# Performance work log

Hardware: AMD Instinct MI355X
Metric: run time of the kernel (lower is better)

The kernel has to match this reference:

```python
import jax, jax.numpy as jnp
import numpy as np

N = 100000
E = 1600000
IN_C, HID, HEADS, OUT_C = 128, 64, 4, 2
NEG_SLOPE = 0.2


def setup_inputs() -> dict:
    key = jax.random.key(0)
    ks = jax.random.split(key, 10)
    def glorot(k, shape):
        fan = shape[0] + shape[-1]
        return jax.random.uniform(k, shape, jnp.float32, -1.0, 1.0) * np.sqrt(6.0 / fan)
    x = jax.random.normal(ks[0], (N, IN_C), jnp.float32)
    edge_index = jax.random.randint(ks[1], (2, E), 0, N, jnp.int64)
    return {
        "x": x,
        "edge_index": edge_index,
        "W1": glorot(ks[2], (IN_C, HID)),
        "b1": jnp.zeros((HID,), jnp.float32),
        "W2": glorot(ks[3], (HID, HEADS * HID)),
        "att_src": glorot(ks[4], (HEADS, HID)) ,
        "att_dst": glorot(ks[5], (HEADS, HID)),
        "b2": jnp.zeros((HEADS * HID,), jnp.float32),
        "W3": glorot(ks[6], (HEADS * HID, OUT_C)),
        "b3": jnp.zeros((OUT_C,), jnp.float32),
    }


def _add_self_loops(edge_index, n):
    loop = jnp.arange(n, dtype=edge_index.dtype)
    src = jnp.concatenate([edge_index[0], loop])
    dst = jnp.concatenate([edge_index[1], loop])
    return src, dst


def gcn_conv(x, W, b, src, dst, n):
    # x' = X W, then symmetric deg-normalized scatter-add (self-loops included)
    xw = x @ W
    deg = jax.ops.segment_sum(jnp.ones_like(dst, dtype=xw.dtype), dst, num_segments=n)
    dinv = jnp.where(deg > 0, jax.lax.rsqrt(deg), 0.0)
    norm = dinv[src] * dinv[dst]                      # [E2]
    out = jax.ops.segment_sum(xw[src] * norm[:, None], dst, num_segments=n)
    return out + b


def gat_conv(x, W, att_src, att_dst, b, src, dst, n, heads, ch):
    xw = (x @ W).reshape(n, heads, ch)                # [N, H, C]
    a_s = (xw * att_src).sum(-1)                      # [N, H]
    a_d = (xw * att_dst).sum(-1)
    e = jax.nn.leaky_relu(a_s[src] + a_d[dst], NEG_SLOPE)   # [E2, H]
    # segment softmax over incoming edges per destination node
    m = jax.ops.segment_max(e, dst, num_segments=n)
    m = jnp.where(jnp.isfinite(m), m, 0.0)
    e = jnp.exp(e - m[dst])
    den = jax.ops.segment_sum(e, dst, num_segments=n)
    alpha = e / (den[dst] + 1e-16)                    # [E2, H]
    out = jax.ops.segment_sum(xw[src] * alpha[:, :, None], dst, num_segments=n)
    return out.reshape(n, heads * ch) + b


def reference(x, edge_index, W1, b1, W2, att_src, att_dst, b2, W3, b3):
    n = x.shape[0]
    src, dst = _add_self_loops(edge_index, n)
    h = jax.nn.relu(gcn_conv(x, W1, b1, src, dst, n))
    h = jax.nn.elu(gat_conv(h, W2, att_src, att_dst, b2, src, dst, n, HEADS, HID))
    return gcn_conv(h, W3, b3, src, dst, n)
```

## Files before the change

### kernel.cpp

```cpp
#include <hip/hip_runtime.h>
#include <math.h>

#define N_NODES 100000
#define N_EDGES 1600000
#define E2      (N_NODES + N_EDGES)
#define IN_C    128
#define HID     64
#define HEADS   4
#define HH      256
#define OUT_C   2
#define NEG_SLOPE 0.2f

#define SB   1024
#define NSB  ((N_NODES + SB - 1) / SB)
#define NCHUNK 6250
#define NRANGE 8
#define RDIV   12500
#define RT     10
#define NT1    6250
#define NGB    1563
#define NHG    (NCHUNK + NGB)

typedef __attribute__((ext_vector_type(8))) short bf16x8;
typedef __attribute__((ext_vector_type(4))) float f32x4;

__device__ __forceinline__ float bf2f(unsigned short u) {
    return __uint_as_float(((unsigned)u) << 16);
}
__device__ __forceinline__ unsigned short f2bf(float f) {
    unsigned u = __float_as_uint(f);
    u += 0x7fffu + ((u >> 16) & 1u);
    return (unsigned short)(u >> 16);
}


__global__ __launch_bounds__(256) void k_prep(const float* __restrict__ W2,
        const float* __restrict__ W1,
        const float* __restrict__ att_src, const float* __restrict__ att_dst,
        unsigned short* __restrict__ W2t, unsigned short* __restrict__ wsdt,
        unsigned short* __restrict__ W1t, int* __restrict__ cnt) {
    int b = blockIdx.x, t = threadIdx.x;
    if (b < 64) {
        int g = b * 256 + t;
        int k = g >> 8, n = g & 255;
        W2t[n * 64 + k] = f2bf(W2[g]);
        return;
    }
    if (b < 66) {
        int g = (b - 64) * 256 + t;
        wsdt[512 + g] = 0;
        int k = g >> 3, o = g & 7;
        int h = o & 3;
        const float* att = (o < 4) ? att_src : att_dst;
        float acc = 0.f;
        const float* wrow = W2 + (size_t)k * HH + h * 64;
        const float* arow = att + h * 64;
        for (int c = 0; c < 64; ++c) acc = fmaf(wrow[c], arow[c], acc);
        wsdt[o * 64 + k] = f2bf(acc);
        return;
    }
    if (b < 98) {
        int g = (b - 66) * 256 + t;
        int k = g >> 6, n = g & 63;
        W1t[n * 128 + k] = f2bf(W1[g]);
        return;
    }
    int i = ((b - 98) * 256 + t) * 4;
    if (i + 3 < N_NODES) *(int4*)(cnt + i) = make_int4(0, 0, 0, 0);
    else for (int k = 0; k < 4; ++k) if (i + k < N_NODES) cnt[i + k] = 0;
}

__global__ __launch_bounds__(256) void k_hg(const int* __restrict__ ei,
        int* __restrict__ cnt, int* __restrict__ rank,
        const float* __restrict__ x, const unsigned short* __restrict__ W1t,
        unsigned short* __restrict__ xw1b) {
    int b = blockIdx.x;
    if (b % 5 == 2) {
        int t = threadIdx.x;
        int lane = t & 63, wv = t >> 6;
        int m = lane & 15, quad = lane >> 4;
        bf16x8 B[4][4];
#pragma unroll
        for (int ct = 0; ct < 4; ++ct)
#pragma unroll
            for (int ks = 0; ks < 4; ++ks)
                B[ct][ks] = *(const bf16x8*)(W1t + (size_t)(ct * 16 + m) * IN_C
                                             + ks * 32 + quad * 8);
        int tile = (b / 5) * 4 + wv;
        if (tile >= NT1) return;
        int rbase = tile * 16;
        const float* xp = x + (size_t)(rbase + m) * IN_C + quad * 8;
        f32x4 c0 = {0.f, 0.f, 0.f, 0.f}, c1 = c0, c2 = c0, c3 = c0;
#pragma unroll
        for (int ks = 0; ks < 4; ++ks) {
            float4 f0 = *(const float4*)(xp + ks * 32);
            float4 f1 = *(const float4*)(xp + ks * 32 + 4);
            bf16x8 a;
            a[0] = (short)f2bf(f0.x); a[1] = (short)f2bf(f0.y);
            a[2] = (short)f2bf(f0.z); a[3] = (short)f2bf(f0.w);
            a[4] = (short)f2bf(f1.x); a[5] = (short)f2bf(f1.y);
            a[6] = (short)f2bf(f1.z); a[7] = (short)f2bf(f1.w);
            c0 = __builtin_amdgcn_mfma_f32_16x16x32_bf16(a, B[0][ks], c0, 0, 0, 0);
            c1 = __builtin_amdgcn_mfma_f32_16x16x32_bf16(a, B[1][ks], c1, 0, 0, 0);
            c2 = __builtin_amdgcn_mfma_f32_16x16x32_bf16(a, B[2][ks], c2, 0, 0, 0);
            c3 = __builtin_amdgcn_mfma_f32_16x16x32_bf16(a, B[3][ks], c3, 0, 0, 0);
        }
        int row0 = rbase + quad * 4;
#pragma unroll
        for (int ct = 0; ct < 4; ++ct) {
            f32x4 c = (ct == 0) ? c0 : (ct == 1) ? c1 : (ct == 2) ? c2 : c3;
            unsigned short* p = xw1b + (size_t)row0 * HID + ct * 16 + m;
#pragma unroll
            for (int r = 0; r < 4; ++r) p[(size_t)r * HID] = f2bf(c[r]);
        }
        return;
    }
    int hb = b - (b + 2) / 5;
    int i = hb * 256 + threadIdx.x;
    rank[i] = atomicAdd(&cnt[ei[N_EDGES + i]], 1);
}

__global__ __launch_bounds__(256) void k_scan1(const int* __restrict__ cnt,
                                               int* __restrict__ bsum) {
    int b = blockIdx.x, t = threadIdx.x;
    int i = b * SB + t * 4;
    int s = 0;
    if (i + 3 < N_NODES) {
        int4 v = *(const int4*)(cnt + i);
        s = (v.x + v.y) + (v.z + v.w) + 4;
    } else {
        for (int k = 0; k < 4; ++k) if (i + k < N_NODES) s += cnt[i + k] + 1;
    }
#pragma unroll
    for (int off = 1; off < 64; off <<= 1) s += __shfl_xor(s, off);
    __shared__ int wsum[4];
    int lane = t & 63, wv = t >> 6;
    if (lane == 0) wsum[wv] = s;
    __syncthreads();
    if (t == 0) bsum[b] = (wsum[0] + wsum[1]) + (wsum[2] + wsum[3]);
}

__global__ __launch_bounds__(256) void k_scan3(const int* __restrict__ cnt,
        const int* __restrict__ bsum, int* __restrict__ rowptr,
        float* __restrict__ dinv, int* __restrict__ col) {
    int b = blockIdx.x, t = threadIdx.x;
    int lane = t & 63, wv = t >> 6;
    __shared__ int wred[4];
    {
        int v = (t < b) ? bsum[t] : 0;
#pragma unroll
        for (int off = 1; off < 64; off <<= 1) v += __shfl_xor(v, off);
        if (lane == 0) wred[wv] = v;
    }
    __syncthreads();
    int pre = (wred[0] + wred[1]) + (wred[2] + wred[3]);
    __syncthreads();

    int i = b * SB + t * 4;
    int c0 = 0, c1 = 0, c2 = 0, c3 = 0;
    if (i + 3 < N_NODES) {
        int4 v = *(const int4*)(cnt + i);
        c0 = v.x; c1 = v.y; c2 = v.z; c3 = v.w;
    } else if (i < N_NODES) {
        c0 = cnt[i];
        if (i + 1 < N_NODES) c1 = cnt[i + 1];
        if (i + 2 < N_NODES) c2 = cnt[i + 2];
    }
    int n0 = (i < N_NODES), n1 = (i + 1 < N_NODES),
        n2 = (i + 2 < N_NODES), n3 = (i + 3 < N_NODES);
    int d0 = c0 + n0, d1 = c1 + n1, d2 = c2 + n2, d3 = c3 + n3;
    int s = (d0 + d1) + (d2 + d3);
    int inc = s;
#pragma unroll
    for (int off = 1; off < 64; off <<= 1) {
        int u = __shfl_up(inc, off);
        if (lane >= off) inc += u;
    }
    __shared__ int wtot[4];
    if (lane == 63) wtot[wv] = inc;
    __syncthreads();
    int base = pre + (inc - s);
    for (int w = 0; w < wv; ++w) base += wtot[w];
    if (n0) { rowptr[i]     = base;                dinv[i]     = rsqrtf((float)d0); col[base] = i; }
    if (n1) { rowptr[i + 1] = base + d0;           dinv[i + 1] = rsqrtf((float)d1); col[base + d0] = i + 1; }
    if (n2) { rowptr[i + 2] = base + d0 + d1;      dinv[i + 2] = rsqrtf((float)d2); col[base + d0 + d1] = i + 2; }
    if (n3) { rowptr[i + 3] = base + d0 + d1 + d2; dinv[i + 3] = rsqrtf((float)d3); col[base + d0 + d1 + d2] = i + 3; }
    if (b == 0 && t == 0) rowptr[N_NODES] = E2;
}

__global__ void k_fill(const int* __restrict__ ei, const int* __restrict__ rowptr,
                       const int* __restrict__ rank, int* __restrict__ col) {
    int r = blockIdx.x / NCHUNK;
    int c = blockIdx.x - r * NCHUNK;
    int i = c * 256 + threadIdx.x;
    int d = ei[N_EDGES + i];
    if (d / RDIV != r) return;
    col[rowptr[d] + 1 + rank[i]] = ei[i];
}

__global__ __launch_bounds__(256) void k_agg1(const int* __restrict__ rowptr,
        const int* __restrict__ col, const unsigned short* __restrict__ xw1b,
        const float* __restrict__ dinv, const float* __restrict__ b1,
        unsigned short* __restrict__ h1b) {
    int t = threadIdx.x;
    int lane = t & 63;
    int d = blockIdx.x * 4 + (t >> 6);
    if (d >= N_NODES) return;
    int start = rowptr[d], end = rowptr[d + 1];
    int sub = lane >> 4;
    int cpos = lane & 15;
    float4 acc = make_float4(0.f, 0.f, 0.f, 0.f);
    for (int base = start; base < end; base += 64) {
        int cnt = min(64, end - base);
        int sl = (base + lane < end) ? col[base + lane] : 0;
#pragma unroll 2
        for (int j = 0; j < cnt; j += 4) {
            int idx = j + sub;
            int sj = __shfl(sl, idx);
            if (idx < cnt) {
                float di = dinv[sj];
                ushort4 v = ((const ushort4*)(xw1b + (size_t)sj * HID))[cpos];
                acc.x = fmaf(di, bf2f(v.x), acc.x);
                acc.y = fmaf(di, bf2f(v.y), acc.y);
                acc.z = fmaf(di, bf2f(v.z), acc.z);
                acc.w = fmaf(di, bf2f(v.w), acc.w);
            }
        }
    }
    acc.x += __shfl_xor(acc.x, 16); acc.y += __shfl_xor(acc.y, 16);
    acc.z += __shfl_xor(acc.z, 16); acc.w += __shfl_xor(acc.w, 16);
    acc.x += __shfl_xor(acc.x, 32); acc.y += __shfl_xor(acc.y, 32);
    acc.z += __shfl_xor(acc.z, 32); acc.w += __shfl_xor(acc.w, 32);
    if (lane < 16) {
        float di = dinv[d];
        float4 b = ((const float4*)b1)[lane];
        float ox = fmaf(acc.x, di, b.x); ox = ox > 0.f ? ox : 0.f;
        float oy = fmaf(acc.y, di, b.y); oy = oy > 0.f ? oy : 0.f;
        float oz = fmaf(acc.z, di, b.z); oz = oz > 0.f ? oz : 0.f;
        float ow = fmaf(acc.w, di, b.w); ow = ow > 0.f ? ow : 0.f;
        ushort4 o = make_ushort4(f2bf(ox), f2bf(oy), f2bf(oz), f2bf(ow));
        ((ushort4*)(h1b + (size_t)d * HID))[lane] = o;
    }
}

__global__ __launch_bounds__(256) void k_attn(const unsigned short* __restrict__ h1b,
        const unsigned short* __restrict__ wsdt,
        float* __restrict__ a_s, float* __restrict__ a_d) {
    int t = threadIdx.x;
    int lane = t & 63, wv = t >> 6;
    int m = lane & 15, quad = lane >> 4;
    bf16x8 Bw0 = *(const bf16x8*)(wsdt + (size_t)m * 64 + quad * 8);
    bf16x8 Bw1 = *(const bf16x8*)(wsdt + (size_t)m * 64 + 32 + quad * 8);
    int tile = blockIdx.x * 4 + wv;
    if (tile >= NT1) return;
    int rbase = tile * 16;
    const unsigned short* ap = h1b + (size_t)(rbase + m) * 64 + quad * 8;
    bf16x8 a0 = *(const bf16x8*)(ap);
    bf16x8 a1 = *(const bf16x8*)(ap + 32);
    f32x4 aw = {0.f, 0.f, 0.f, 0.f};
    aw = __builtin_amdgcn_mfma_f32_16x16x32_bf16(a0, Bw0, aw, 0, 0, 0);
    aw = __builtin_amdgcn_mfma_f32_16x16x32_bf16(a1, Bw1, aw, 0, 0, 0);
    int row = rbase + quad * 4;
    if (m < 4) {
#pragma unroll
        for (int r = 0; r < 4; ++r) a_s[(row + r) * 4 + m] = aw[r];
    } else if (m < 8) {
#pragma unroll
        for (int r = 0; r < 4; ++r) a_d[(row + r) * 4 + (m - 4)] = aw[r];
    }
}

__global__ __launch_bounds__(256) void k_agg2u(const int* __restrict__ rowptr,
        const int* __restrict__ col, const unsigned short* __restrict__ h1b,
        const float* __restrict__ a_s, const float* __restrict__ a_d,
        unsigned short* __restrict__ ub, int dbase) {
    __shared__ int   ss[4][64];
    __shared__ float sp[4][64][4];
    int t = threadIdx.x;
    int lane = t & 63, wv = t >> 6;
    int d = dbase + blockIdx.x * 4 + wv;
    if (d >= N_NODES) return;
    const float4* as4 = (const float4*)a_s;
    float4 adv = ((const float4*)a_d)[d];
    int start = rowptr[d], end = rowptr[d + 1];

    float den0 = 0.f, den1 = 0.f, den2 = 0.f, den3 = 0.f;
    float acc0 = 0.f, acc1 = 0.f, acc2 = 0.f, acc3 = 0.f;
    for (int base = start; base < end; base += 64) {
        int cnt = min(64, end - base);
        float p0 = 0.f, p1 = 0.f, p2 = 0.f, p3 = 0.f;
        int s = 0;
        if (lane < cnt) {
            s = col[base + lane];
            float4 av = as4[s];
            float v;
            v = av.x + adv.x; v = v > 0.f ? v : NEG_SLOPE * v; p0 = __expf(v);
            v = av.y + adv.y; v = v > 0.f ? v : NEG_SLOPE * v; p1 = __expf(v);
            v = av.z + adv.z; v = v > 0.f ? v : NEG_SLOPE * v; p2 = __expf(v);
            v = av.w + adv.w; v = v > 0.f ? v : NEG_SLOPE * v; p3 = __expf(v);
            den0 += p0; den1 += p1; den2 += p2; den3 += p3;
        }
        ss[wv][lane] = s;
        ((float4*)sp[wv])[lane] = make_float4(p0, p1, p2, p3);
#pragma unroll 4
        for (int j = 0; j < cnt; ++j) {
            int sj = ss[wv][j];
            float4 pj = ((const float4*)sp[wv])[j];
            float v = bf2f(h1b[(unsigned)sj * 64u + (unsigned)lane]);
            acc0 = fmaf(pj.x, v, acc0);
            acc1 = fmaf(pj.y, v, acc1);
            acc2 = fmaf(pj.z, v, acc2);
            acc3 = fmaf(pj.w, v, acc3);
        }
    }
#pragma unroll
    for (int mk = 1; mk < 64; mk <<= 1) {
        den0 += __shfl_xor(den0, mk);
        den1 += __shfl_xor(den1, mk);
        den2 += __shfl_xor(den2, mk);
        den3 += __shfl_xor(den3, mk);
    }
    float u0 = acc0 / (den0 + 1e-16f);
    float u1 = acc1 / (den1 + 1e-16f);
    float u2 = acc2 / (den2 + 1e-16f);
    float u3 = acc3 / (den3 + 1e-16f);
    unsigned short* up = ub + (size_t)d * HH;
    up[lane]       = f2bf(u0);
    up[64 + lane]  = f2bf(u1);
    up[128 + lane] = f2bf(u2);
    up[192 + lane] = f2bf(u3);
}

__global__ __launch_bounds__(256) void k_gemm3m(const unsigned short* __restrict__ ub,
        const unsigned short* __restrict__ W2t, const float* __restrict__ b2,
        const float* __restrict__ W3, const float* __restrict__ dinv,
        float2* __restrict__ xw3) {
    int t = threadIdx.x;
    int lane = t & 63, wv = t >> 6;
    int m = lane & 15, quad = lane >> 4;
    int nb = wv * 64 + m;
    bf16x8 B[4][2];
#pragma unroll
    for (int ct = 0; ct < 4; ++ct)
#pragma unroll
        for (int ks = 0; ks < 2; ++ks)
            B[ct][ks] = *(const bf16x8*)(W2t + (size_t)(nb + ct * 16) * 64
                                         + ks * 32 + quad * 8);
    float bv[4]; float2 w3v[4];
#pragma unroll
    for (int ct = 0; ct < 4; ++ct) {
        int n = nb + ct * 16;
        bv[ct] = b2[n];
        w3v[ct] = ((const float2*)W3)[n];
    }
    __shared__ float red[4][16][2];
    int r0 = blockIdx.x * (RT * 16);
    for (int tile = 0; tile < RT; ++tile) {
        int rbase = r0 + tile * 16;
        const unsigned short* ap = ub + (size_t)(rbase + m) * HH + wv * 64 + quad * 8;
        bf16x8 a0 = *(const bf16x8*)(ap);
        bf16x8 a1 = *(const bf16x8*)(ap + 32);
        f32x4 c0 = {0.f, 0.f, 0.f, 0.f}, c1 = c0, c2 = c0, c3 = c0;
        c0 = __builtin_amdgcn_mfma_f32_16x16x32_bf16(a0, B[0][0], c0, 0, 0, 0);
        c1 = __builtin_amdgcn_mfma_f32_16x16x32_bf16(a0, B[1][0], c1, 0, 0, 0);
        c2 = __builtin_amdgcn_mfma_f32_16x16x32_bf16(a0, B[2][0], c2, 0, 0, 0);
        c3 = __builtin_amdgcn_mfma_f32_16x16x32_bf16(a0, B[3][0], c3, 0, 0, 0);
        c0 = __builtin_amdgcn_mfma_f32_16x16x32_bf16(a1, B[0][1], c0, 0, 0, 0);
        c1 = __builtin_amdgcn_mfma_f32_16x16x32_bf16(a1, B[1][1], c1, 0, 0, 0);
        c2 = __builtin_amdgcn_mfma_f32_16x16x32_bf16(a1, B[2][1], c2, 0, 0, 0);
        c3 = __builtin_amdgcn_mfma_f32_16x16x32_bf16(a1, B[3][1], c3, 0, 0, 0);
        float px[4] = {0.f, 0.f, 0.f, 0.f}, py[4] = {0.f, 0.f, 0.f, 0.f};
#pragma unroll
        for (int ct = 0; ct < 4; ++ct) {
            f32x4 c = (ct == 0) ? c0 : (ct == 1) ? c1 : (ct == 2) ? c2 : c3;
#pragma unroll
            for (int r = 0; r < 4; ++r) {
                float o = c[r] + bv[ct];
                o = o > 0.f ? o : expm1f(o);
                px[r] = fmaf(o, w3v[ct].x, px[r]);
                py[r] = fmaf(o, w3v[ct].y, py[r]);
            }
        }
#pragma unroll
        for (int mk = 1; mk < 16; mk <<= 1) {
#pragma unroll
            for (int r = 0; r < 4; ++r) {
                px[r] += __shfl_xor(px[r], mk);
                py[r] += __shfl_xor(py[r], mk);
            }
        }
        if (m == 0) {
#pragma unroll
            for (int r = 0; r < 4; ++r) {
                red[wv][quad * 4 + r][0] = px[r];
                red[wv][quad * 4 + r][1] = py[r];
            }
        }
        __syncthreads();
        if (t < 32) {
            int row = t >> 1, xy = t & 1;
            float s = red[0][row][xy] + red[1][row][xy]
                    + red[2][row][xy] + red[3][row][xy];
            ((float*)(xw3 + (rbase + row)))[xy] = s * dinv[rbase + row];
        }
        __syncthreads();
    }
}

__global__ __launch_bounds__(256) void k_agg3(const int* __restrict__ rowptr,
        const int* __restrict__ col, const float2* __restrict__ xw3,
        const float* __restrict__ dinv, const float* __restrict__ b3,
        float* __restrict__ out) {
    int t = threadIdx.x;
    int lane = t & 63;
    int g = lane >> 2, s = lane & 3;
    int d = blockIdx.x * 64 + (t >> 6) * 16 + g;
    if (d >= N_NODES) return;
    int e0 = rowptr[d], e1 = rowptr[d + 1];
    float a0 = 0.f, a1 = 0.f;
    for (int e = e0 + s; e < e1; e += 4) {
        float2 v = xw3[col[e]];
        a0 += v.x; a1 += v.y;
    }
    a0 += __shfl_xor(a0, 1); a1 += __shfl_xor(a1, 1);
    a0 += __shfl_xor(a0, 2); a1 += __shfl_xor(a1, 2);
    if (s == 0) {
        float di = dinv[d];
        out[d * 2 + 0] = fmaf(a0, di, b3[0]);
        out[d * 2 + 1] = fmaf(a1, di, b3[1]);
    }
}


extern "C" void kernel_launch(void* const* d_in, const int* in_sizes, int n_in,
                              void* d_out, int out_size, void* d_ws, size_t ws_size,
                              hipStream_t stream) {
    const float* x       = (const float*)d_in[0];
    const int*   ei      = (const int*)d_in[1];
    const float* W1      = (const float*)d_in[2];
    const float* b1      = (const float*)d_in[3];
    const float* W2      = (const float*)d_in[4];
    const float* att_src = (const float*)d_in[5];
    const float* att_dst = (const float*)d_in[6];
    const float* b2      = (const float*)d_in[7];
    const float* W3      = (const float*)d_in[8];
    const float* b3      = (const float*)d_in[9];
    float* out = (float*)d_out;
    (void)in_sizes; (void)n_in; (void)out_size; (void)ws_size;

    char* ws = (char*)d_ws;
    size_t off = 0;
    auto alloc = [&](size_t bytes) -> void* {
        void* p = ws + off;
        off = (off + bytes + 255) & ~(size_t)255;
        return p;
    };
    int*    rowptr = (int*)alloc((N_NODES + 1) * sizeof(int));
    int*    cnt    = (int*)alloc(N_NODES * sizeof(int));
    int*    bsum   = (int*)alloc(NSB * sizeof(int));
    int*    rank   = (int*)alloc((size_t)N_EDGES * sizeof(int));
    int*    col    = (int*)alloc((size_t)E2 * sizeof(int));
    float*  dinv   = (float*)alloc(N_NODES * sizeof(float));
    unsigned short* W2t  = (unsigned short*)alloc(64 * 256 * sizeof(unsigned short));
    unsigned short* wsdt = (unsigned short*)alloc(16 * 64 * sizeof(unsigned short));
    unsigned short* W1t  = (unsigned short*)alloc(64 * 128 * sizeof(unsigned short));
    unsigned short* xw1b = (unsigned short*)alloc((size_t)N_NODES * HID * sizeof(unsigned short));
    unsigned short* h1b  = (unsigned short*)alloc((size_t)N_NODES * HID * sizeof(unsigned short));
    float*  a_s    = (float*)alloc((size_t)N_NODES * HEADS * sizeof(float));
    float*  a_d    = (float*)alloc((size_t)N_NODES * HEADS * sizeof(float));
    unsigned short* ub   = (unsigned short*)alloc((size_t)N_NODES * HH * sizeof(unsigned short));
    float2* xw3    = (float2*)alloc((size_t)N_NODES * sizeof(float2));

    k_prep<<<196, 256, 0, stream>>>(W2, W1, att_src, att_dst, W2t, wsdt, W1t, cnt);
    k_hg<<<NHG, 256, 0, stream>>>(ei, cnt, rank, x, W1t, xw1b);
    k_scan1<<<NSB, 256, 0, stream>>>(cnt, bsum);
    k_scan3<<<NSB, 256, 0, stream>>>(cnt, bsum, rowptr, dinv, col);
    k_fill<<<NCHUNK * NRANGE, 256, 0, stream>>>(ei, rowptr, rank, col);

    k_agg1<<<(N_NODES + 3) / 4, 256, 0, stream>>>(rowptr, col, xw1b, dinv, b1, h1b);
    k_attn<<<(NT1 + 3) / 4, 256, 0, stream>>>(h1b, wsdt, a_s, a_d);
    const int HALF = 50000;
    k_agg2u<<<HALF / 4, 256, 0, stream>>>(rowptr, col, h1b, a_s, a_d, ub, 0);
    k_agg2u<<<(N_NODES - HALF + 3) / 4, 256, 0, stream>>>(rowptr, col, h1b, a_s, a_d, ub, HALF);
    k_gemm3m<<<(N_NODES / 16) / RT, 256, 0, stream>>>(ub, W2t, b2, W3, dinv, xw3);
    k_agg3<<<(N_NODES + 63) / 64, 256, 0, stream>>>(rowptr, col, xw3, dinv, b3, out);
}
```

Baseline: 382.1 us.

## Build CSR with per-chunk shared-memory histograms instead of global atomic ranks

Replaces the global per-edge atomicAdd rank pass and rank-based fill with a two-pass blocked counting sort. Each block builds a shared-memory histogram for one (destination range, edge chunk) pair and stores it as 16-bit counts in scratch space borrowed from the ub buffer. The scan kernel turns these into per-chunk exclusive offsets and node counts, and the fill pass uses shared-memory atomics to place each source. This removes contended global atomics and the 6.4MB rank array. In exchange the edge list is re-read once per destination range in both passes, and edges within a bucket are no longer placed in a deterministic order.

```diff
diff --git a/kernel.cpp b/kernel.cpp
--- a/kernel.cpp
+++ b/kernel.cpp
@@ -13,13 +13,16 @@
 
 #define SB   1024
 #define NSB  ((N_NODES + SB - 1) / SB)
-#define NCHUNK 6250
 #define NRANGE 8
 #define RDIV   12500
+#define BINS   RDIV
+#define NBK    100
+#define CHUNK  (N_EDGES / NBK)
+#define CITER  ((CHUNK + 255) / 256)
+#define NHB    (NRANGE * NBK)
 #define RT     10
 #define NT1    6250
-#define NGB    1563
-#define NHG    (NCHUNK + NGB)
+#define NGEMM1 ((NT1 + 3) / 4)
 
 typedef __attribute__((ext_vector_type(8))) short bf16x8;
 typedef __attribute__((ext_vector_type(4))) float f32x4;
@@ -38,7 +41,7 @@
         const float* __restrict__ W1,
         const float* __restrict__ att_src, const float* __restrict__ att_dst,
         unsigned short* __restrict__ W2t, unsigned short* __restrict__ wsdt,
-        unsigned short* __restrict__ W1t, int* __restrict__ cnt) {
+        unsigned short* __restrict__ W1t) {
     int b = blockIdx.x, t = threadIdx.x;
     if (b < 64) {
         int g = b * 256 + t;
@@ -59,77 +62,92 @@
         wsdt[o * 64 + k] = f2bf(acc);
         return;
     }
-    if (b < 98) {
-        int g = (b - 66) * 256 + t;
-        int k = g >> 6, n = g & 63;
-        W1t[n * 128 + k] = f2bf(W1[g]);
-        return;
-    }
-    int i = ((b - 98) * 256 + t) * 4;
-    if (i + 3 < N_NODES) *(int4*)(cnt + i) = make_int4(0, 0, 0, 0);
-    else for (int k = 0; k < 4; ++k) if (i + k < N_NODES) cnt[i + k] = 0;
-}
-
-__global__ __launch_bounds__(256) void k_hg(const int* __restrict__ ei,
-        int* __restrict__ cnt, int* __restrict__ rank,
+    int g = (b - 66) * 256 + t;
+    int k = g >> 6, n = g & 63;
+    W1t[n * 128 + k] = f2bf(W1[g]);
+}
+
+__global__ __launch_bounds__(256) void k_hista(const int* __restrict__ ei,
+        unsigned short* __restrict__ hp16,
         const float* __restrict__ x, const unsigned short* __restrict__ W1t,
         unsigned short* __restrict__ xw1b) {
-    int b = blockIdx.x;
-    if (b % 5 == 2) {
-        int t = threadIdx.x;
-        int lane = t & 63, wv = t >> 6;
-        int m = lane & 15, quad = lane >> 4;
-        bf16x8 B[4][4];
-#pragma unroll
-        for (int ct = 0; ct < 4; ++ct)
-#pragma unroll
-            for (int ks = 0; ks < 4; ++ks)
-                B[ct][ks] = *(const bf16x8*)(W1t + (size_t)(ct * 16 + m) * IN_C
-                                             + ks * 32 + quad * 8);
-        int tile = (b / 5) * 4 + wv;
-        if (tile >= NT1) return;
-        int rbase = tile * 16;
-        const float* xp = x + (size_t)(rbase + m) * IN_C + quad * 8;
-        f32x4 c0 = {0.f, 0.f, 0.f, 0.f}, c1 = c0, c2 = c0, c3 = c0;
-#pragma unroll
-        for (int ks = 0; ks < 4; ++ks) {
-            float4 f0 = *(const float4*)(xp + ks * 32);
-            float4 f1 = *(const float4*)(xp + ks * 32 + 4);
-            bf16x8 a;
-            a[0] = (short)f2bf(f0.x); a[1] = (short)f2bf(f0.y);
-            a[2] = (short)f2bf(f0.z); a[3] = (short)f2bf(f0.w);
-            a[4] = (short)f2bf(f1.x); a[5] = (short)f2bf(f1.y);
-            a[6] = (short)f2bf(f1.z); a[7] = (short)f2bf(f1.w);
-            c0 = __builtin_amdgcn_mfma_f32_16x16x32_bf16(a, B[0][ks], c0, 0, 0, 0);
-            c1 = __builtin_amdgcn_mfma_f32_16x16x32_bf16(a, B[1][ks], c1, 0, 0, 0);
-            c2 = __builtin_amdgcn_mfma_f32_16x16x32_bf16(a, B[2][ks], c2, 0, 0, 0);
-            c3 = __builtin_amdgcn_mfma_f32_16x16x32_bf16(a, B[3][ks], c3, 0, 0, 0);
-        }
-        int row0 = rbase + quad * 4;
-#pragma unroll
-        for (int ct = 0; ct < 4; ++ct) {
-            f32x4 c = (ct == 0) ? c0 : (ct == 1) ? c1 : (ct == 2) ? c2 : c3;
-            unsigned short* p = xw1b + (size_t)row0 * HID + ct * 16 + m;
-#pragma unroll
-            for (int r = 0; r < 4; ++r) p[(size_t)r * HID] = f2bf(c[r]);
-        }
+    __shared__ unsigned int hh[BINS];
+    int b = blockIdx.x, t = threadIdx.x;
+    if (b < NHB) {
+        int r = b / NBK, k = b - r * NBK;
+        for (int i = t; i < BINS; i += 256) hh[i] = 0u;
+        __syncthreads();
+        const int* dp = ei + N_EDGES + (size_t)k * CHUNK;
+        int lo = r * RDIV;
+        for (int it = 0; it < CITER; ++it) {
+            int idx = it * 256 + t;
+            if (idx < CHUNK) {
+                int d = dp[idx] - lo;
+                if ((unsigned)d < (unsigned)RDIV) atomicAdd(&hh[d], 1u);
+            }
+        }
+        __syncthreads();
+        unsigned short* hp = hp16 + (size_t)b * BINS;
+        for (int i = t; i < BINS; i += 256) hp[i] = (unsigned short)hh[i];
         return;
     }
-    int hb = b - (b + 2) / 5;
-    int i = hb * 256 + threadIdx.x;
-    rank[i] = atomicAdd(&cnt[ei[N_EDGES + i]], 1);
-}
-
-__global__ __launch_bounds__(256) void k_scan1(const int* __restrict__ cnt,
-                                               int* __restrict__ bsum) {
+    int lane = t & 63, wv = t >> 6;
+    int m = lane & 15, quad = lane >> 4;
+    bf16x8 B[4][4];
+#pragma unroll
+    for (int ct = 0; ct < 4; ++ct)
+#pragma unroll
+        for (int ks = 0; ks < 4; ++ks)
+            B[ct][ks] = *(const bf16x8*)(W1t + (size_t)(ct * 16 + m) * IN_C
+                                         + ks * 32 + quad * 8);
+    int tile = (b - NHB) * 4 + wv;
+    if (tile >= NT1) return;
+    int rbase = tile * 16;
+    const float* xp = x + (size_t)(rbase + m) * IN_C + quad * 8;
+    f32x4 c0 = {0.f, 0.f, 0.f, 0.f}, c1 = c0, c2 = c0, c3 = c0;
+#pragma unroll
+    for (int ks = 0; ks < 4; ++ks) {
+        float4 f0 = *(const float4*)(xp + ks * 32);
+        float4 f1 = *(const float4*)(xp + ks * 32 + 4);
+        bf16x8 a;
+        a[0] = (short)f2bf(f0.x); a[1] = (short)f2bf(f0.y);
+        a[2] = (short)f2bf(f0.z); a[3] = (short)f2bf(f0.w);
+        a[4] = (short)f2bf(f1.x); a[5] = (short)f2bf(f1.y);
+        a[6] = (short)f2bf(f1.z); a[7] = (short)f2bf(f1.w);
+        c0 = __builtin_amdgcn_mfma_f32_16x16x32_bf16(a, B[0][ks], c0, 0, 0, 0);
+        c1 = __builtin_amdgcn_mfma_f32_16x16x32_bf16(a, B[1][ks], c1, 0, 0, 0);
+        c2 = __builtin_amdgcn_mfma_f32_16x16x32_bf16(a, B[2][ks], c2, 0, 0, 0);
+        c3 = __builtin_amdgcn_mfma_f32_16x16x32_bf16(a, B[3][ks], c3, 0, 0, 0);
+    }
+    int row0 = rbase + quad * 4;
+#pragma unroll
+    for (int ct = 0; ct < 4; ++ct) {
+        f32x4 c = (ct == 0) ? c0 : (ct == 1) ? c1 : (ct == 2) ? c2 : c3;
+        unsigned short* p = xw1b + (size_t)row0 * HID + ct * 16 + m;
+#pragma unroll
+        for (int r = 0; r < 4; ++r) p[(size_t)r * HID] = f2bf(c[r]);
+    }
+}
+
+__global__ __launch_bounds__(256) void k_scan1(unsigned short* __restrict__ hp16,
+        int* __restrict__ cnt, int* __restrict__ bsum) {
     int b = blockIdx.x, t = threadIdx.x;
-    int i = b * SB + t * 4;
     int s = 0;
-    if (i + 3 < N_NODES) {
-        int4 v = *(const int4*)(cnt + i);
-        s = (v.x + v.y) + (v.z + v.w) + 4;
-    } else {
-        for (int k = 0; k < 4; ++k) if (i + k < N_NODES) s += cnt[i + k] + 1;
+#pragma unroll
+    for (int u = 0; u < 4; ++u) {
+        int i = b * SB + u * 256 + t;
+        if (i < N_NODES) {
+            int r = i / RDIV, bin = i - r * RDIV;
+            unsigned short* p = hp16 + (size_t)r * NBK * BINS + bin;
+            unsigned acc = 0;
+            for (int k = 0; k < NBK; ++k) {
+                unsigned short hv = p[(size_t)k * BINS];
+                p[(size_t)k * BINS] = (unsigned short)acc;
+                acc += hv;
+            }
+            cnt[i] = (int)acc;
+            s += (int)acc + 1;
+        }
     }
 #pragma unroll
     for (int off = 1; off < 64; off <<= 1) s += __shfl_xor(s, off);
@@ -188,14 +206,29 @@
     if (b == 0 && t == 0) rowptr[N_NODES] = E2;
 }
 
-__global__ void k_fill(const int* __restrict__ ei, const int* __restrict__ rowptr,
-                       const int* __restrict__ rank, int* __restrict__ col) {
-    int r = blockIdx.x / NCHUNK;
-    int c = blockIdx.x - r * NCHUNK;
-    int i = c * 256 + threadIdx.x;
-    int d = ei[N_EDGES + i];
-    if (d / RDIV != r) return;
-    col[rowptr[d] + 1 + rank[i]] = ei[i];
+__global__ __launch_bounds__(256) void k_fillb(const int* __restrict__ ei,
+        const int* __restrict__ rowptr, const unsigned short* __restrict__ hp16,
+        int* __restrict__ col) {
+    __shared__ unsigned int cur[BINS];
+    int b = blockIdx.x, t = threadIdx.x;
+    int r = b / NBK, k = b - r * NBK;
+    int lo = r * RDIV;
+    const unsigned short* pp = hp16 + (size_t)b * BINS;
+    for (int i = t; i < BINS; i += 256)
+        cur[i] = (unsigned)rowptr[lo + i] + 1u + (unsigned)pp[i];
+    __syncthreads();
+    const int* dp = ei + N_EDGES + (size_t)k * CHUNK;
+    const int* sp = ei + (size_t)k * CHUNK;
+    for (int it = 0; it < CITER; ++it) {
+        int idx = it * 256 + t;
+        if (idx < CHUNK) {
+            int d = dp[idx] - lo;
+            if ((unsigned)d < (unsigned)RDIV) {
+                unsigned pos = atomicAdd(&cur[d], 1u);
+                col[pos] = sp[idx];
+            }
+        }
+    }
 }
 
 __global__ __launch_bounds__(256) void k_agg1(const int* __restrict__ rowptr,
@@ -458,7 +491,6 @@
     int*    rowptr = (int*)alloc((N_NODES + 1) * sizeof(int));
     int*    cnt    = (int*)alloc(N_NODES * sizeof(int));
     int*    bsum   = (int*)alloc(NSB * sizeof(int));
-    int*    rank   = (int*)alloc((size_t)N_EDGES * sizeof(int));
     int*    col    = (int*)alloc((size_t)E2 * sizeof(int));
     float*  dinv   = (float*)alloc(N_NODES * sizeof(float));
     unsigned short* W2t  = (unsigned short*)alloc(64 * 256 * sizeof(unsigned short));
@@ -470,12 +502,13 @@
     float*  a_d    = (float*)alloc((size_t)N_NODES * HEADS * sizeof(float));
     unsigned short* ub   = (unsigned short*)alloc((size_t)N_NODES * HH * sizeof(unsigned short));
     float2* xw3    = (float2*)alloc((size_t)N_NODES * sizeof(float2));
-
-    k_prep<<<196, 256, 0, stream>>>(W2, W1, att_src, att_dst, W2t, wsdt, W1t, cnt);
-    k_hg<<<NHG, 256, 0, stream>>>(ei, cnt, rank, x, W1t, xw1b);
-    k_scan1<<<NSB, 256, 0, stream>>>(cnt, bsum);
+    unsigned short* hp16 = ub;
+
+    k_prep<<<98, 256, 0, stream>>>(W2, W1, att_src, att_dst, W2t, wsdt, W1t);
+    k_hista<<<NHB + NGEMM1, 256, 0, stream>>>(ei, hp16, x, W1t, xw1b);
+    k_scan1<<<NSB, 256, 0, stream>>>(hp16, cnt, bsum);
     k_scan3<<<NSB, 256, 0, stream>>>(cnt, bsum, rowptr, dinv, col);
-    k_fill<<<NCHUNK * NRANGE, 256, 0, stream>>>(ei, rowptr, rank, col);
+    k_fillb<<<NHB, 256, 0, stream>>>(ei, rowptr, hp16, col);
 
     k_agg1<<<(N_NODES + 3) / 4, 256, 0, stream>>>(rowptr, col, xw1b, dinv, b1, h1b);
     k_attn<<<(NT1 + 3) / 4, 256, 0, stream>>>(h1b, wsdt, a_s, a_d);
```

Measured after the change: 426.5 us. 11.6% more time.
